# Kernel tuning notes

Measured on AMD Instinct MI355X. Metric: run time of the kernel, lower is better.

The kernel has to match this reference:

```python
import jax, jax.numpy as jnp
import numpy as np

N_NODES = 100000
N_EDGES = 3200000
IN_C = 256
OUT_C = 64
NEG_SLOPE = 0.2  # leaky_relu alpha


def setup_inputs() -> dict:
    key = jax.random.key(0)
    k1, k2, k3, k4 = jax.random.split(key, 4)
    x = jax.random.normal(k1, (N_NODES, IN_C), dtype=jnp.float32)
    edge_index = jax.random.randint(k2, (2, N_EDGES), 0, N_NODES, dtype=jnp.int32)
    # xavier-ish scales
    W = jax.random.normal(k3, (OUT_C, IN_C), dtype=jnp.float32) * (1.0 / np.sqrt(IN_C))
    a = jax.random.normal(k4, (2 * OUT_C, 1), dtype=jnp.float32) * 0.1
    return {"x": x, "edge_index": edge_index, "W": W, "a": a, "num_nodes": N_NODES}


def reference(x, edge_index, W, a, num_nodes):
    # eval mode: dropout is identity
    # add self loops
    loop = jnp.arange(num_nodes, dtype=edge_index.dtype)
    row = jnp.concatenate([edge_index[0], loop])  # source nodes (x_j)
    col = jnp.concatenate([edge_index[1], loop])  # destination nodes (x_i)

    h = x @ W.T  # [N, out_c]

    # e = cat([x_i, x_j], 1) @ a  ==  (h @ a_i)[col] + (h @ a_j)[row]
    a_i = a[:OUT_C, 0]
    a_j = a[OUT_C:, 0]
    s_i = h @ a_i  # [N]
    s_j = h @ a_j  # [N]
    e = jax.nn.leaky_relu(s_i[col] + s_j[row], negative_slope=NEG_SLOPE)  # [E+N]

    # segment softmax over destination node (col)
    m = jax.ops.segment_max(e, col, num_segments=num_nodes)  # [N]
    ex = jnp.exp(e - m[col])
    denom = jax.ops.segment_sum(ex, col, num_segments=num_nodes)  # [N]
    alpha = ex / denom[col]  # [E+N]

    # scatter-add aggregation: out[col] += alpha * h[row]
    out = jax.ops.segment_sum(alpha[:, None] * h[row], col, num_segments=num_nodes)
    return out
```

## Files before the change

kernel.cpp:

```cpp
#include <hip/hip_runtime.h>
#include <hip/hip_bf16.h>
#include <cstddef>
#include <cstdint>

#define IN_C 256
#define OUT_C 64
#define NEG_SLOPE 0.2f
#define BKT2 256
#define PCHUNK 4096
#define MAXB 512
#define CAP 9728

typedef __attribute__((ext_vector_type(4))) float f32x4;
typedef __attribute__((ext_vector_type(2))) float f32x2;
typedef __attribute__((ext_vector_type(8))) short s16x8;

__device__ __forceinline__ ushort f2bf(float f)
{
    uint32_t u = __float_as_uint(f);
    u += 0x7fffu + ((u >> 16) & 1u);
    return (ushort)(u >> 16);
}

__device__ __forceinline__ uint32_t pack_bf2(float f0, float f1)
{
    const uint32_t u0 = __float_as_uint(f0) + 0x8000u;
    const uint32_t u1 = __float_as_uint(f1) + 0x8000u;
    return (u1 & 0xffff0000u) | (u0 >> 16);
}

__global__ __launch_bounds__(256) void wconv_kernel(
    const float* __restrict__ W, ushort* __restrict__ wfrag,
    int* __restrict__ cursor, int nb)
{
    if (blockIdx.x == 64) {
        for (int i = threadIdx.x; i < nb; i += 256) cursor[i] = i * CAP;
        return;
    }
    const int idx = blockIdx.x * 256 + threadIdx.x;
    const int j = idx & 7;
    const int l = (idx >> 3) & 63;
    const int n = (idx >> 9) & 3;
    const int t = idx >> 11;
    const int k   = t * 32 + ((l >> 4) << 3) + j;
    const int col = n * 16 + (l & 15);
    wfrag[idx] = f2bf(W[col * IN_C + k]);
}

__global__ __launch_bounds__(256) void fused_h_mfma(
    const float* __restrict__ x, const ushort* __restrict__ wfrag,
    const float* __restrict__ a, ushort* __restrict__ hb,
    float* __restrict__ s_i, float* __restrict__ s_j, int n_nodes)
{
    __shared__ ushort Bs[32 * 64 * 8];

    const int tid = threadIdx.x;
    for (int i = tid; i < 2048; i += 256)
        ((float4*)Bs)[i] = ((const float4*)wfrag)[i];
    __syncthreads();

    const int lane = tid & 63;
    const int wv   = tid >> 6;
    const int m    = lane & 15;
    const int quad = lane >> 4;

    const int base = blockIdx.x * 64 + wv * 16;
    int row = base + m;
    if (row >= n_nodes) row = n_nodes - 1;

    f32x4 acc0 = {0.f, 0.f, 0.f, 0.f};
    f32x4 acc1 = {0.f, 0.f, 0.f, 0.f};
    f32x4 acc2 = {0.f, 0.f, 0.f, 0.f};
    f32x4 acc3 = {0.f, 0.f, 0.f, 0.f};

    const float* xrow = x + (size_t)row * IN_C + quad * 8;

    #pragma unroll
    for (int t = 0; t < 8; ++t) {
        const float4 xa = *(const float4*)(xrow + t * 32);
        const float4 xb = *(const float4*)(xrow + t * 32 + 4);
        union { s16x8 v; uint32_t u[4]; } af;
        af.u[0] = pack_bf2(xa.x, xa.y);
        af.u[1] = pack_bf2(xa.z, xa.w);
        af.u[2] = pack_bf2(xb.x, xb.y);
        af.u[3] = pack_bf2(xb.z, xb.w);

        const s16x8 b0 = *(const s16x8*)(Bs + ((t * 4 + 0) * 64 + lane) * 8);
        const s16x8 b1 = *(const s16x8*)(Bs + ((t * 4 + 1) * 64 + lane) * 8);
        const s16x8 b2 = *(const s16x8*)(Bs + ((t * 4 + 2) * 64 + lane) * 8);
        const s16x8 b3 = *(const s16x8*)(Bs + ((t * 4 + 3) * 64 + lane) * 8);

        acc0 = __builtin_amdgcn_mfma_f32_16x16x32_bf16(af.v, b0, acc0, 0, 0, 0);
        acc1 = __builtin_amdgcn_mfma_f32_16x16x32_bf16(af.v, b1, acc1, 0, 0, 0);
        acc2 = __builtin_amdgcn_mfma_f32_16x16x32_bf16(af.v, b2, acc2, 0, 0, 0);
        acc3 = __builtin_amdgcn_mfma_f32_16x16x32_bf16(af.v, b3, acc3, 0, 0, 0);
    }

    const int c0 = lane & 15;
    const float ai0 = a[c0],      ai1 = a[c0 + 16], ai2 = a[c0 + 32], ai3 = a[c0 + 48];
    const float aj0 = a[64 + c0], aj1 = a[80 + c0], aj2 = a[96 + c0], aj3 = a[112 + c0];

    #pragma unroll
    for (int r = 0; r < 4; ++r) {
        const int rowr = base + quad * 4 + r;
        float pi = acc0[r] * ai0 + acc1[r] * ai1 + acc2[r] * ai2 + acc3[r] * ai3;
        float pj = acc0[r] * aj0 + acc1[r] * aj1 + acc2[r] * aj2 + acc3[r] * aj3;
        pi += __shfl_xor(pi, 1, 64);  pj += __shfl_xor(pj, 1, 64);
        pi += __shfl_xor(pi, 2, 64);  pj += __shfl_xor(pj, 2, 64);
        pi += __shfl_xor(pi, 4, 64);  pj += __shfl_xor(pj, 4, 64);
        pi += __shfl_xor(pi, 8, 64);  pj += __shfl_xor(pj, 8, 64);
        if (rowr < n_nodes) {
            ushort* hr = hb + (size_t)rowr * OUT_C + c0;
            hr[0]  = f2bf(acc0[r]);
            hr[16] = f2bf(acc1[r]);
            hr[32] = f2bf(acc2[r]);
            hr[48] = f2bf(acc3[r]);
            if (c0 == 0) { s_i[rowr] = pi; s_j[rowr] = pj; }
        }
    }
}

__global__ __launch_bounds__(512) void partition_kernel(
    const int* __restrict__ ei, int* __restrict__ cursor,
    uint32_t* __restrict__ rec, int n_edges, int nb)
{
    __shared__ int      hist[MAXB];
    __shared__ int      lbase[MAXB];
    __shared__ int      gbase[MAXB];
    __shared__ int      lcur[MAXB];
    __shared__ uint32_t srt[PCHUNK];
    __shared__ uint16_t bmap[PCHUNK];

    const int tid  = threadIdx.x;
    const int base = blockIdx.x * PCHUNK;
    const int lim  = min(PCHUNK, n_edges - base);

    hist[tid] = 0;
    __syncthreads();

    int rA[PCHUNK / 512], cA[PCHUNK / 512];
    #pragma unroll
    for (int k = 0; k < PCHUNK / 512; ++k) {
        const int i = tid + (k << 9);
        if (i < lim) {
            rA[k] = __builtin_nontemporal_load(ei + base + i);
            cA[k] = __builtin_nontemporal_load(ei + n_edges + base + i);
            atomicAdd(&hist[(uint32_t)cA[k] >> 8], 1);
        }
    }
    __syncthreads();

    const int v = hist[tid];
    lbase[tid] = v;
    __syncthreads();
    for (int off = 1; off < 512; off <<= 1) {
        const int mine  = lbase[tid];
        const int other = (tid >= off) ? lbase[tid - off] : 0;
        __syncthreads();
        lbase[tid] = mine + other;
        __syncthreads();
    }
    const int excl = lbase[tid] - v;
    __syncthreads();
    lbase[tid] = excl;
    lcur[tid]  = excl;
    gbase[tid] = (tid < nb && v > 0) ? atomicAdd(&cursor[tid], v) : 0;
    __syncthreads();

    #pragma unroll
    for (int k = 0; k < PCHUNK / 512; ++k) {
        const int i = tid + (k << 9);
        if (i < lim) {
            const int r = rA[k];
            const int c = cA[k];
            const int b = (uint32_t)c >> 8;
            const int pos = atomicAdd(&lcur[b], 1);
            srt[pos]  = ((uint32_t)r << 8) | (uint32_t)(c & (BKT2 - 1));
            bmap[pos] = (uint16_t)b;
        }
    }
    __syncthreads();

    for (int i = tid; i < lim; i += 512) {
        const int b = bmap[i];
        rec[gbase[b] + (i - lbase[b])] = srt[i];
    }
}

__global__ __launch_bounds__(1024) void sortgather_kernel(
    const uint32_t* __restrict__ rec, const ushort* __restrict__ hb,
    const float* __restrict__ s_i, const float* __restrict__ s_j,
    const int* __restrict__ cursor, float* __restrict__ out, int n_nodes)
{
    __shared__ uint32_t srt[CAP];
    __shared__ int hcnt[BKT2];
    __shared__ int nstart[BKT2 + 1];
    __shared__ int lcur[BKT2];
    __shared__ int sscan[BKT2];

    const int b     = blockIdx.x;
    const int tid   = threadIdx.x;
    const int start = b * CAP;
    const int cnt   = min(cursor[b] - start, CAP);

    if (tid < BKT2) hcnt[tid] = 0;
    __syncthreads();

    const int cnt4 = cnt >> 2;
    for (int i = tid; i < cnt4; i += 1024) {
        const uint4 rv4 = ((const uint4*)(rec + start))[i];
        atomicAdd(&hcnt[rv4.x & (BKT2 - 1)], 1);
        atomicAdd(&hcnt[rv4.y & (BKT2 - 1)], 1);
        atomicAdd(&hcnt[rv4.z & (BKT2 - 1)], 1);
        atomicAdd(&hcnt[rv4.w & (BKT2 - 1)], 1);
    }
    for (int i = (cnt & ~3) + tid; i < cnt; i += 1024)
        atomicAdd(&hcnt[rec[start + i] & (BKT2 - 1)], 1);
    __syncthreads();

    if (tid < BKT2) sscan[tid] = hcnt[tid];
    __syncthreads();
    for (int off = 1; off < BKT2; off <<= 1) {
        int mine = 0, other = 0;
        if (tid < BKT2) {
            mine  = sscan[tid];
            other = (tid >= off) ? sscan[tid - off] : 0;
        }
        __syncthreads();
        if (tid < BKT2) sscan[tid] = mine + other;
        __syncthreads();
    }
    if (tid < BKT2) {
        const int excl = sscan[tid] - hcnt[tid];
        nstart[tid] = excl;
        lcur[tid]   = excl;
    }
    if (tid == 0) nstart[BKT2] = cnt;
    __syncthreads();

    for (int i = tid; i < cnt; i += 1024) {
        const uint32_t rv = rec[start + i];
        srt[atomicAdd(&lcur[rv & (BKT2 - 1)], 1)] = rv;
    }
    __syncthreads();

    const int lane = tid & 63;
    const int wv   = tid >> 6;
    const int g    = lane >> 3;
    const int l8   = lane & 7;
    const uint32_t loff = (uint32_t)(l8 << 4);
    const char* hbB = (const char*)hb;

    for (int k = 0; k < BKT2 / 16; ++k) {
        const int nl   = wv * (BKT2 / 16) + k;
        const int node = b * BKT2 + nl;
        if (node >= n_nodes) break;
        const int o  = nstart[nl];
        const int oe = nstart[nl + 1];
        const float si = s_i[node];

        f32x2 a01 = {0.f, 0.f}, a23 = {0.f, 0.f};
        f32x2 a45 = {0.f, 0.f}, a67 = {0.f, 0.f};
        float dsum = 0.f;

        int e = o;
        for (; e + 32 <= oe; e += 32) {
            uint32_t rv[4];
            #pragma unroll
            for (int q = 0; q < 4; ++q) rv[q] = srt[e + q * 8 + g];
            float sj[4]; uint32_t off[4];
            #pragma unroll
            for (int q = 0; q < 4; ++q) {
                sj[q]  = s_j[rv[q] >> 8];
                off[q] = ((rv[q] & 0xFFFFFF00u) >> 1) + loff;
            }
            uint4 hv[4];
            #pragma unroll
            for (int q = 0; q < 4; ++q) hv[q] = *(const uint4*)(hbB + off[q]);
            #pragma unroll
            for (int q = 0; q < 4; ++q) {
                const float t  = si + sj[q];
                const float ex = __expf(fmaxf(t, NEG_SLOPE * t));
                const f32x2 e2 = {ex, ex};
                f32x2 h;
                h[0] = __uint_as_float(hv[q].x << 16);
                h[1] = __uint_as_float(hv[q].x & 0xffff0000u);
                a01 += e2 * h;
                h[0] = __uint_as_float(hv[q].y << 16);
                h[1] = __uint_as_float(hv[q].y & 0xffff0000u);
                a23 += e2 * h;
                h[0] = __uint_as_float(hv[q].z << 16);
                h[1] = __uint_as_float(hv[q].z & 0xffff0000u);
                a45 += e2 * h;
                h[0] = __uint_as_float(hv[q].w << 16);
                h[1] = __uint_as_float(hv[q].w & 0xffff0000u);
                a67 += e2 * h;
                dsum += ex;
            }
        }
        for (; e + 8 <= oe; e += 8) {
            const uint32_t rv = srt[e + g];
            const float sjv = s_j[rv >> 8];
            const uint32_t off = ((rv & 0xFFFFFF00u) >> 1) + loff;
            const uint4 hv = *(const uint4*)(hbB + off);
            const float t  = si + sjv;
            const float ex = __expf(fmaxf(t, NEG_SLOPE * t));
            const f32x2 e2 = {ex, ex};
            f32x2 h;
            h[0] = __uint_as_float(hv.x << 16);
            h[1] = __uint_as_float(hv.x & 0xffff0000u);
            a01 += e2 * h;
            h[0] = __uint_as_float(hv.y << 16);
            h[1] = __uint_as_float(hv.y & 0xffff0000u);
            a23 += e2 * h;
            h[0] = __uint_as_float(hv.z << 16);
            h[1] = __uint_as_float(hv.z & 0xffff0000u);
            a45 += e2 * h;
            h[0] = __uint_as_float(hv.w << 16);
            h[1] = __uint_as_float(hv.w & 0xffff0000u);
            a67 += e2 * h;
            dsum += ex;
        }
        if (e < oe) {
            const int m = oe - e;
            const uint32_t rv = srt[e + (g < m ? g : m - 1)];
            const float sjv = s_j[rv >> 8];
            const uint32_t off = ((rv & 0xFFFFFF00u) >> 1) + loff;
            const uint4 hv = *(const uint4*)(hbB + off);
            const float t  = si + sjv;
            const float ex = (g < m) ? __expf(fmaxf(t, NEG_SLOPE * t)) : 0.f;
            const f32x2 e2 = {ex, ex};
            f32x2 h;
            h[0] = __uint_as_float(hv.x << 16);
            h[1] = __uint_as_float(hv.x & 0xffff0000u);
            a01 += e2 * h;
            h[0] = __uint_as_float(hv.y << 16);
            h[1] = __uint_as_float(hv.y & 0xffff0000u);
            a23 += e2 * h;
            h[0] = __uint_as_float(hv.z << 16);
            h[1] = __uint_as_float(hv.z & 0xffff0000u);
            a45 += e2 * h;
            h[0] = __uint_as_float(hv.w << 16);
            h[1] = __uint_as_float(hv.w & 0xffff0000u);
            a67 += e2 * h;
            dsum += ex;
        }

        #pragma unroll
        for (int s = 8; s <= 32; s <<= 1) {
            a01[0] += __shfl_xor(a01[0], s, 64);
            a01[1] += __shfl_xor(a01[1], s, 64);
            a23[0] += __shfl_xor(a23[0], s, 64);
            a23[1] += __shfl_xor(a23[1], s, 64);
            a45[0] += __shfl_xor(a45[0], s, 64);
            a45[1] += __shfl_xor(a45[1], s, 64);
            a67[0] += __shfl_xor(a67[0], s, 64);
            a67[1] += __shfl_xor(a67[1], s, 64);
            dsum   += __shfl_xor(dsum,   s, 64);
        }

        const float t0  = si + s_j[node];
        const float ex0 = __expf(fmaxf(t0, NEG_SLOPE * t0));
        const uint4 hs = *(const uint4*)(hbB + (size_t)node * 128 + loff);
        a01[0] += ex0 * __uint_as_float(hs.x << 16);
        a01[1] += ex0 * __uint_as_float(hs.x & 0xffff0000u);
        a23[0] += ex0 * __uint_as_float(hs.y << 16);
        a23[1] += ex0 * __uint_as_float(hs.y & 0xffff0000u);
        a45[0] += ex0 * __uint_as_float(hs.z << 16);
        a45[1] += ex0 * __uint_as_float(hs.z & 0xffff0000u);
        a67[0] += ex0 * __uint_as_float(hs.w << 16);
        a67[1] += ex0 * __uint_as_float(hs.w & 0xffff0000u);
        dsum += ex0;

        if (g == 0) {
            const float inv = 1.0f / dsum;
            f32x4 o4;
            o4[0] = a01[0] * inv;
            o4[1] = a01[1] * inv;
            o4[2] = a23[0] * inv;
            o4[3] = a23[1] * inv;
            float* op = out + (size_t)node * OUT_C + (l8 << 3);
            __builtin_nontemporal_store(o4, (f32x4*)op);
            o4[0] = a45[0] * inv;
            o4[1] = a45[1] * inv;
            o4[2] = a67[0] * inv;
            o4[3] = a67[1] * inv;
            __builtin_nontemporal_store(o4, (f32x4*)(op + 4));
        }
    }
}

extern "C" void kernel_launch(void* const* d_in, const int* in_sizes, int n_in,
                              void* d_out, int out_size, void* d_ws, size_t ws_size,
                              hipStream_t stream)
{
    const float* x  = (const float*)d_in[0];
    const int*   ei = (const int*)d_in[1];
    const float* W  = (const float*)d_in[2];
    const float* a  = (const float*)d_in[3];

    const int N  = in_sizes[0] / IN_C;
    const int E  = in_sizes[1] / 2;
    const int NB = (N + BKT2 - 1) / BKT2;

    float* out = (float*)d_out;

    char* ws = (char*)d_ws;
    ushort* hb      = (ushort*)ws;                ws += (size_t)N * OUT_C * 2;
    float*  s_i     = (float*)ws;                 ws += (size_t)N * 4;
    float*  s_j     = (float*)ws;                 ws += (size_t)N * 4;
    int*    cursor  = (int*)ws;                   ws += (size_t)MAXB * 4;
    ws = (char*)(((uintptr_t)ws + 15) & ~(uintptr_t)15);
    ushort* wfrag   = (ushort*)ws;                ws += 32 * 64 * 8 * 2;
    ws = (char*)(((uintptr_t)ws + 15) & ~(uintptr_t)15);
    uint32_t* rec   = (uint32_t*)ws;

    hipLaunchKernelGGL(wconv_kernel, dim3(65), dim3(256), 0, stream,
                       W, wfrag, cursor, NB);
    hipLaunchKernelGGL(fused_h_mfma, dim3((N + 63) / 64), dim3(256), 0, stream,
                       x, wfrag, a, hb, s_i, s_j, N);

    const int pblocks = (E + PCHUNK - 1) / PCHUNK;
    hipLaunchKernelGGL(partition_kernel, dim3(pblocks), dim3(512), 0, stream,
                       ei, cursor, rec, E, NB);

    hipLaunchKernelGGL(sortgather_kernel, dim3(NB), dim3(1024), 0, stream,
                       rec, hb, s_i, s_j, cursor, out, N);
}
```

Baseline: 280.2 us.

## Merge projection GEMM and edge partition into one heterogeneous launch

Combines the MFMA projection kernel and the edge bucket-partition kernel into a single launch. The first PB blocks do partitioning and the remaining blocks do the projection, so the two independent stages run at the same time and one launch boundary disappears. The partition path moves from 512 to 256 threads, handles two histogram bins per thread, and replaces the barrier-heavy Hillis-Steele scan with a wave-shuffle scan. Both paths share a 32 KB shared buffer, which may lower occupancy for the projection blocks.

```diff
diff --git a/kernel.cpp b/kernel.cpp
--- a/kernel.cpp
+++ b/kernel.cpp
@@ -47,14 +47,95 @@
     wfrag[idx] = f2bf(W[col * IN_C + k]);
 }
 
-__global__ __launch_bounds__(256) void fused_h_mfma(
+__global__ __launch_bounds__(256) void fused_proj_part(
     const float* __restrict__ x, const ushort* __restrict__ wfrag,
     const float* __restrict__ a, ushort* __restrict__ hb,
-    float* __restrict__ s_i, float* __restrict__ s_j, int n_nodes)
-{
-    __shared__ ushort Bs[32 * 64 * 8];
+    float* __restrict__ s_i, float* __restrict__ s_j, int n_nodes,
+    const int* __restrict__ ei, int* __restrict__ cursor,
+    uint32_t* __restrict__ rec, int n_edges, int nb, int pb)
+{
+    __shared__ __align__(16) char smem[32 * 1024];
+    __shared__ int wtot[4];
 
     const int tid = threadIdx.x;
+
+    if ((int)blockIdx.x < pb) {
+        int* hist  = (int*)smem;
+        int* lbase = (int*)(smem + 2048);
+        int* gbase = (int*)(smem + 4096);
+        int* lcur  = (int*)(smem + 6144);
+        uint32_t* srt  = (uint32_t*)(smem + 8192);
+        uint16_t* bmap = (uint16_t*)(smem + 24576);
+
+        const int base = blockIdx.x * PCHUNK;
+        const int lim  = min(PCHUNK, n_edges - base);
+
+        hist[tid] = 0;
+        hist[tid + 256] = 0;
+        __syncthreads();
+
+        int rA[PCHUNK / 256], cA[PCHUNK / 256];
+        #pragma unroll
+        for (int k = 0; k < PCHUNK / 256; ++k) {
+            const int i = tid + (k << 8);
+            if (i < lim) {
+                rA[k] = __builtin_nontemporal_load(ei + base + i);
+                cA[k] = __builtin_nontemporal_load(ei + n_edges + base + i);
+                atomicAdd(&hist[(uint32_t)cA[k] >> 8], 1);
+            }
+        }
+        __syncthreads();
+
+        const int h0 = hist[2 * tid];
+        const int h1 = hist[2 * tid + 1];
+        const int pv = h0 + h1;
+        const int lane = tid & 63;
+        const int w    = tid >> 6;
+        int incl = pv;
+        #pragma unroll
+        for (int d = 1; d < 64; d <<= 1) {
+            const int o = __shfl_up(incl, d, 64);
+            if (lane >= d) incl += o;
+        }
+        if (lane == 63) wtot[w] = incl;
+        __syncthreads();
+        int wpre = 0;
+        for (int q = 0; q < w; ++q) wpre += wtot[q];
+        const int excl_pair = incl + wpre - pv;
+
+        lbase[2 * tid]     = excl_pair;
+        lbase[2 * tid + 1] = excl_pair + h0;
+        lcur[2 * tid]      = excl_pair;
+        lcur[2 * tid + 1]  = excl_pair + h0;
+        gbase[2 * tid]     = (2 * tid < nb && h0 > 0)
+                             ? atomicAdd(&cursor[2 * tid], h0) : 0;
+        gbase[2 * tid + 1] = (2 * tid + 1 < nb && h1 > 0)
+                             ? atomicAdd(&cursor[2 * tid + 1], h1) : 0;
+        __syncthreads();
+
+        #pragma unroll
+        for (int k = 0; k < PCHUNK / 256; ++k) {
+            const int i = tid + (k << 8);
+            if (i < lim) {
+                const int r = rA[k];
+                const int c = cA[k];
+                const int b = (uint32_t)c >> 8;
+                const int pos = atomicAdd(&lcur[b], 1);
+                srt[pos]  = ((uint32_t)r << 8) | (uint32_t)(c & (BKT2 - 1));
+                bmap[pos] = (uint16_t)b;
+            }
+        }
+        __syncthreads();
+
+        for (int i = tid; i < lim; i += 256) {
+            const int b = bmap[i];
+            rec[gbase[b] + (i - lbase[b])] = srt[i];
+        }
+        return;
+    }
+
+    ushort* Bs = (ushort*)smem;
+
     for (int i = tid; i < 2048; i += 256)
         ((float4*)Bs)[i] = ((const float4*)wfrag)[i];
     __syncthreads();
@@ -64,7 +145,7 @@
     const int m    = lane & 15;
     const int quad = lane >> 4;
 
-    const int base = blockIdx.x * 64 + wv * 16;
+    const int base = (blockIdx.x - pb) * 64 + wv * 16;
     int row = base + m;
     if (row >= n_nodes) row = n_nodes - 1;
 
@@ -117,73 +198,6 @@
             hr[48] = f2bf(acc3[r]);
             if (c0 == 0) { s_i[rowr] = pi; s_j[rowr] = pj; }
         }
-    }
-}
-
-__global__ __launch_bounds__(512) void partition_kernel(
-    const int* __restrict__ ei, int* __restrict__ cursor,
-    uint32_t* __restrict__ rec, int n_edges, int nb)
-{
-    __shared__ int      hist[MAXB];
-    __shared__ int      lbase[MAXB];
-    __shared__ int      gbase[MAXB];
-    __shared__ int      lcur[MAXB];
-    __shared__ uint32_t srt[PCHUNK];
-    __shared__ uint16_t bmap[PCHUNK];
-
-    const int tid  = threadIdx.x;
-    const int base = blockIdx.x * PCHUNK;
-    const int lim  = min(PCHUNK, n_edges - base);
-
-    hist[tid] = 0;
-    __syncthreads();
-
-    int rA[PCHUNK / 512], cA[PCHUNK / 512];
-    #pragma unroll
-    for (int k = 0; k < PCHUNK / 512; ++k) {
-        const int i = tid + (k << 9);
-        if (i < lim) {
-            rA[k] = __builtin_nontemporal_load(ei + base + i);
-            cA[k] = __builtin_nontemporal_load(ei + n_edges + base + i);
-            atomicAdd(&hist[(uint32_t)cA[k] >> 8], 1);
-        }
-    }
-    __syncthreads();
-
-    const int v = hist[tid];
-    lbase[tid] = v;
-    __syncthreads();
-    for (int off = 1; off < 512; off <<= 1) {
-        const int mine  = lbase[tid];
-        const int other = (tid >= off) ? lbase[tid - off] : 0;
-        __syncthreads();
-        lbase[tid] = mine + other;
-        __syncthreads();
-    }
-    const int excl = lbase[tid] - v;
-    __syncthreads();
-    lbase[tid] = excl;
-    lcur[tid]  = excl;
-    gbase[tid] = (tid < nb && v > 0) ? atomicAdd(&cursor[tid], v) : 0;
-    __syncthreads();
-
-    #pragma unroll
-    for (int k = 0; k < PCHUNK / 512; ++k) {
-        const int i = tid + (k << 9);
-        if (i < lim) {
-            const int r = rA[k];
-            const int c = cA[k];
-            const int b = (uint32_t)c >> 8;
-            const int pos = atomicAdd(&lcur[b], 1);
-            srt[pos]  = ((uint32_t)r << 8) | (uint32_t)(c & (BKT2 - 1));
-            bmap[pos] = (uint16_t)b;
-        }
-    }
-    __syncthreads();
-
-    for (int i = tid; i < lim; i += 512) {
-        const int b = bmap[i];
-        rec[gbase[b] + (i - lbase[b])] = srt[i];
     }
 }
 
@@ -417,12 +431,12 @@
 
     hipLaunchKernelGGL(wconv_kernel, dim3(65), dim3(256), 0, stream,
                        W, wfrag, cursor, NB);
-    hipLaunchKernelGGL(fused_h_mfma, dim3((N + 63) / 64), dim3(256), 0, stream,
-                       x, wfrag, a, hb, s_i, s_j, N);
-
-    const int pblocks = (E + PCHUNK - 1) / PCHUNK;
-    hipLaunchKernelGGL(partition_kernel, dim3(pblocks), dim3(512), 0, stream,
-                       ei, cursor, rec, E, NB);
+
+    const int PB = (E + PCHUNK - 1) / PCHUNK;
+    const int MB = (N + 63) / 64;
+    hipLaunchKernelGGL(fused_proj_part, dim3(PB + MB), dim3(256), 0, stream,
+                       x, wfrag, a, hb, s_i, s_j, N,
+                       ei, cursor, rec, E, NB, PB);
 
     hipLaunchKernelGGL(sortgather_kernel, dim3(NB), dim3(1024), 0, stream,
                        rec, hb, s_i, s_j, cursor, out, N);
```

Measured after the change: 287.5 us. 1.03x slower.
